# Performance work log

Hardware: AMD Instinct MI355X
Metric: run time of the kernel (lower is better)

Reference implementation:

```python
import jax, jax.numpy as jnp
import numpy as np

WS = 8
NH = 6

def _ln(x, g, b, eps=1e-5):
    m = x.mean(-1, keepdims=True)
    v = jnp.var(x, axis=-1, keepdims=True)
    return (x - m) / jnp.sqrt(v + eps) * g + b

def _dwconv(x_nchw, k):
    # depthwise 3x3, stride 1, padding 1 (SAME); k: (C,1,3,3)
    return jax.lax.conv_general_dilated(
        x_nchw, k, (1, 1), 'SAME',
        dimension_numbers=('NCHW', 'OIHW', 'NCHW'),
        feature_group_count=x_nchw.shape[1])

def setup_inputs() -> dict:
    key = jax.random.key(0)
    ks = jax.random.split(key, 12)
    B, H, W, C = 2, 256, 256, 180
    hd_ffn = 360
    s = 0.02
    return {
        'x': jax.random.normal(ks[0], (B, H * W, C), jnp.float32),
        'w_qkv': jax.random.normal(ks[1], (3 * C, C), jnp.float32) * s,
        'b_rel': jax.random.normal(ks[2], (NH, WS * WS, WS * WS), jnp.float32) * s,
        'w_proj': jax.random.normal(ks[3], (C, C), jnp.float32) * s,
        'b_proj': jnp.zeros((C,), jnp.float32),
        'conv_dw': jax.random.normal(ks[4], (C, 1, 3, 3), jnp.float32) * 0.1,
        'cg_w1': jax.random.normal(ks[5], (C // 8, C), jnp.float32) * s,
        'cg_w2': jax.random.normal(ks[6], (C, C // 8), jnp.float32) * s,
        'ffn_w1': jax.random.normal(ks[7], (hd_ffn, C), jnp.float32) * s,
        'ffn_dw': jax.random.normal(ks[8], (hd_ffn, 1, 3, 3), jnp.float32) * 0.1,
        'ffn_w2': jax.random.normal(ks[9], (C, hd_ffn), jnp.float32) * s,
        'n1_g': jnp.ones((C,), jnp.float32),
        'n1_b': jnp.zeros((C,), jnp.float32),
        'n2_g': jnp.ones((C,), jnp.float32),
        'n2_b': jnp.zeros((C,), jnp.float32),
        'H': H,
        'W': W,
    }

def reference(x, w_qkv, b_rel, w_proj, b_proj, conv_dw, cg_w1, cg_w2,
              ffn_w1, ffn_dw, ffn_w2, n1_g, n1_b, n2_g, n2_b, H, W):
    B, L, C = x.shape
    hd = C // NH
    scale = hd ** -0.5
    n1 = _ln(x, n1_g, n1_b)
    # --- spatial window attention branch ---
    xw = n1.reshape(B, H // WS, WS, W // WS, WS, C)
    xw = xw.transpose(0, 1, 3, 2, 4, 5).reshape(-1, WS * WS, C)  # (nw, 64, C)
    qkv = (xw @ w_qkv.T).reshape(-1, WS * WS, 3, NH, hd).transpose(2, 0, 3, 1, 4)
    q, k, v = qkv[0], qkv[1], qkv[2]  # (nw, nh, 64, hd)
    attn = jax.nn.softmax((q * scale) @ jnp.swapaxes(k, -2, -1) + b_rel, axis=-1)
    out = (attn @ v).transpose(0, 2, 1, 3).reshape(-1, WS * WS, C)
    out = out @ w_proj.T + b_proj
    attn_feat = out.reshape(B, H // WS, W // WS, WS, WS, C)
    attn_feat = attn_feat.transpose(0, 1, 3, 2, 4, 5).reshape(B, L, C)
    # --- conv branch: depthwise 3x3 + GELU ---
    nchw = n1.transpose(0, 2, 1).reshape(B, C, H, W)
    conv_feat = jax.nn.gelu(_dwconv(nchw, conv_dw), approximate=False)
    conv_feat = conv_feat.reshape(B, C, L).transpose(0, 2, 1)
    # --- AIM: channel gate on conv_feat modulates attn_feat ---
    pooled = conv_feat.mean(axis=1)  # (B, C) == AdaptiveAvgPool2d(1)
    cm = jax.nn.sigmoid(jax.nn.gelu(pooled @ cg_w1.T, approximate=False) @ cg_w2.T)
    x = x + (attn_feat * cm[:, None, :] + conv_feat)
    # --- FFN with depthwise spatial mixing ---
    n2 = _ln(x, n2_g, n2_b)
    h = jax.nn.gelu(n2 @ ffn_w1.T, approximate=False)  # (B, L, hd_ffn)
    hdim = h.shape[-1]
    h_s = _dwconv(h.transpose(0, 2, 1).reshape(B, hdim, H, W), ffn_dw)
    h_s = h_s.reshape(B, hdim, L).transpose(0, 2, 1)
    return x + h_s @ ffn_w2.T
```

## Files before the change

### kernel.cpp

```cpp
#include <hip/hip_runtime.h>
#include <hip/hip_bf16.h>
#include <math.h>

#define BATCH 2
#define IMG 256
#define LTOK 65536
#define CH 180
#define BL (BATCH * LTOK)
#define HDF 360

using frag_ab = __attribute__((ext_vector_type(8))) short;
using frag_cd = __attribute__((ext_vector_type(4))) float;

__device__ __forceinline__ float b2f(unsigned short u) {
    union { unsigned int i; float f; } v; v.i = ((unsigned int)u) << 16; return v.f;
}
__device__ __forceinline__ float blo(unsigned int u) {
    union { unsigned int i; float f; } v; v.i = u << 16; return v.f;
}
__device__ __forceinline__ float bhi(unsigned int u) {
    union { unsigned int i; float f; } v; v.i = u & 0xffff0000u; return v.f;
}
__device__ __forceinline__ unsigned short f2b(float f) {
    union { float f; unsigned int i; } v; v.f = f;
    unsigned int x = v.i;
    unsigned int r = (x + 0x7fffu + ((x >> 16) & 1u)) >> 16;
    return (unsigned short)r;
}
__device__ __forceinline__ float gelu_f(float x) {
    return 0.5f * x * (1.0f + erff(x * 0.70710678118654752f));
}

__global__ __launch_bounds__(256) void convw_kernel(
    const float* __restrict__ a, const float* __restrict__ b,
    const float* __restrict__ c, const float* __restrict__ d,
    const float* __restrict__ cdw, const float* __restrict__ fdw,
    unsigned short* __restrict__ wbf, float* __restrict__ wT1, float* __restrict__ wT2)
{
    int g = blockIdx.x * 256 + threadIdx.x;
    if (g < 259200) {
        float v;
        if      (g < 97200)  v = a[g];
        else if (g < 129600) v = b[g - 97200];
        else if (g < 194400) v = c[g - 129600];
        else                 v = d[g - 194400];
        wbf[g] = f2b(v);
    } else if (g < 265680) {
        int i = g - 259200;
        int tap = i / 180, ch = i % 180;
        wT1[i] = cdw[ch * 9 + tap];
    } else if (g < 278640) {
        int i = g - 265680;
        int tap = i / 360, ch = i % 360;
        wT2[i] = fdw[ch * 9 + tap];
    }
}

__device__ __forceinline__ void ld4(const float* p, float v[4]) {
    float4 t = *(const float4*)p; v[0]=t.x; v[1]=t.y; v[2]=t.z; v[3]=t.w;
}
__device__ __forceinline__ void ld4(const unsigned short* p, float v[4]) {
    ushort4 t = *(const ushort4*)p; v[0]=b2f(t.x); v[1]=b2f(t.y); v[2]=b2f(t.z); v[3]=b2f(t.w);
}

template <typename TIN>
__global__ __launch_bounds__(256) void ln_kernel(
    const TIN* __restrict__ x, const float* __restrict__ g,
    const float* __restrict__ bta, unsigned short* __restrict__ out)
{
    int wave = threadIdx.x >> 6, lane = threadIdx.x & 63;
    int tok = blockIdx.x * 4 + wave;
    const bool act = lane < 45;
    float v[4] = {0.f, 0.f, 0.f, 0.f};
    const TIN* row = x + (size_t)tok * CH;
    if (act) ld4(row + lane * 4, v);
    float s  = v[0] + v[1] + v[2] + v[3];
    float sq = v[0]*v[0] + v[1]*v[1] + v[2]*v[2] + v[3]*v[3];
    #pragma unroll
    for (int off = 32; off > 0; off >>= 1) {
        s  += __shfl_xor(s, off);
        sq += __shfl_xor(sq, off);
    }
    float mean = s * (1.f / CH);
    float var  = sq * (1.f / CH) - mean * mean;
    float rstd = rsqrtf(var + 1e-5f);
    if (act) {
        float4 gg = *(const float4*)&g[lane * 4];
        float4 bb = *(const float4*)&bta[lane * 4];
        unsigned int o0 = (unsigned int)f2b((v[0]-mean)*rstd*gg.x + bb.x)
                        | ((unsigned int)f2b((v[1]-mean)*rstd*gg.y + bb.y) << 16);
        unsigned int o1 = (unsigned int)f2b((v[2]-mean)*rstd*gg.z + bb.z)
                        | ((unsigned int)f2b((v[3]-mean)*rstd*gg.w + bb.w) << 16);
        *(uint2*)(out + (size_t)tok * CH + lane * 4) = make_uint2(o0, o1);
    }
}

__device__ __forceinline__ void stv(float* p, float v) { *p = v; }
__device__ __forceinline__ void stv(unsigned short* p, float v) { *p = f2b(v); }

template <int ACT, bool HAS_BIAS, bool HAS_RES, typename TOUT>
__global__ __launch_bounds__(256) void gemm_kernel(
    const unsigned short* __restrict__ X, int ldx,
    const unsigned short* __restrict__ Wt,
    const float* __restrict__ bias,
    const unsigned short* __restrict__ res, int ldr,
    TOUT* __restrict__ Y, int ldy,
    int N, int K)
{
    __shared__ unsigned short Xs[64][40];
    __shared__ unsigned short Ws[64][40];
    const int tid = threadIdx.x;
    const int wave = tid >> 6;
    const int lane = tid & 63;
    const int l16 = lane & 15;
    const int q = lane >> 4;
    const int m0 = blockIdx.x * 64;
    const int n0 = blockIdx.y * 64;
    const int lr = tid >> 2;
    const int lk = (tid & 3) << 3;

    frag_cd acc[4];
    #pragma unroll
    for (int i = 0; i < 4; ++i) acc[i] = (frag_cd){0.f, 0.f, 0.f, 0.f};

    for (int k0 = 0; k0 < K; k0 += 32) {
        const bool kfull = (k0 + 32 <= K);
        {
            const unsigned short* p = X + (size_t)(m0 + lr) * ldx + (k0 + lk);
            if (kfull) {
                *(uint2*)&Xs[lr][lk]     = *(const uint2*)p;
                *(uint2*)&Xs[lr][lk + 4] = *(const uint2*)(p + 4);
            } else {
                #pragma unroll
                for (int j = 0; j < 8; ++j)
                    Xs[lr][lk + j] = (k0 + lk + j < K) ? p[j] : (unsigned short)0;
            }
        }
        {
            const int n = n0 + lr;
            const unsigned short* p = Wt + (size_t)n * K + (k0 + lk);
            if (n < N && kfull) {
                *(uint2*)&Ws[lr][lk]     = *(const uint2*)p;
                *(uint2*)&Ws[lr][lk + 4] = *(const uint2*)(p + 4);
            } else {
                #pragma unroll
                for (int j = 0; j < 8; ++j)
                    Ws[lr][lk + j] = (n < N && (k0 + lk + j) < K) ? p[j] : (unsigned short)0;
            }
        }
        __syncthreads();
        frag_ab bfr = *(const frag_ab*)&Ws[wave * 16 + l16][q * 8];
        #pragma unroll
        for (int mb = 0; mb < 4; ++mb) {
            frag_ab afr = *(const frag_ab*)&Xs[mb * 16 + l16][q * 8];
            acc[mb] = __builtin_amdgcn_mfma_f32_16x16x32_bf16(afr, bfr, acc[mb], 0, 0, 0);
        }
        __syncthreads();
    }
    const int col = n0 + wave * 16 + l16;
    if (col < N) {
        float bv = 0.f;
        if (HAS_BIAS) bv = bias[col];
        #pragma unroll
        for (int mb = 0; mb < 4; ++mb) {
            #pragma unroll
            for (int r = 0; r < 4; ++r) {
                int row = m0 + mb * 16 + q * 4 + r;
                float v = acc[mb][r] + bv;
                if (ACT == 1) v = gelu_f(v);
                if (HAS_RES) v += b2f(res[(size_t)row * ldr + col]);
                stv(&Y[(size_t)row * ldy + col], v);
            }
        }
    }
}

__global__ __launch_bounds__(256) void attn_kernel(
    const unsigned short* __restrict__ qkv,
    const float* __restrict__ b_rel,
    unsigned short* __restrict__ attn_out)
{
    __shared__ float qs[64][33], ks[64][33], vs[64][33];
    __shared__ float S[64][65];
    const int tid = threadIdx.x;
    const int wid = blockIdx.x;
    const int b = wid >> 10;
    const int wy = (wid & 1023) >> 5;
    const int wx = wid & 31;
    const float scale = 0.18257418583505536f;
    const int ty = tid >> 4, tx = tid & 15;

    for (int h = 0; h < 6; ++h) {
        for (int idx = tid; idx < 64 * 32; idx += 256) {
            int r = idx >> 5, d = idx & 31;
            float qv = 0.f, kv = 0.f, vv = 0.f;
            if (d < 30) {
                int l = ((wy << 3) + (r >> 3)) * IMG + (wx << 3) + (r & 7);
                const unsigned short* rowp = qkv + (size_t)(b * LTOK + l) * 540 + h * 30 + d;
                qv = b2f(rowp[0]); kv = b2f(rowp[180]); vv = b2f(rowp[360]);
            }
            qs[r][d] = qv; ks[r][d] = kv; vs[r][d] = vv;
        }
        __syncthreads();
        {
            float a4[4][4] = {{0.f}};
            for (int d = 0; d < 30; ++d) {
                float qv[4], kv[4];
                #pragma unroll
                for (int i = 0; i < 4; ++i) qv[i] = qs[ty * 4 + i][d];
                #pragma unroll
                for (int j = 0; j < 4; ++j) kv[j] = ks[tx * 4 + j][d];
                #pragma unroll
                for (int i = 0; i < 4; ++i)
                    #pragma unroll
                    for (int j = 0; j < 4; ++j) a4[i][j] += qv[i] * kv[j];
            }
            #pragma unroll
            for (int i = 0; i < 4; ++i)
                #pragma unroll
                for (int j = 0; j < 4; ++j) {
                    int ii = ty * 4 + i, jj = tx * 4 + j;
                    S[ii][jj] = a4[i][j] * scale + b_rel[h * 4096 + ii * 64 + jj];
                }
        }
        __syncthreads();
        if (tid < 64) {
            float mx = -1e30f;
            for (int j = 0; j < 64; ++j) mx = fmaxf(mx, S[tid][j]);
            float sum = 0.f;
            for (int j = 0; j < 64; ++j) { float e = __expf(S[tid][j] - mx); S[tid][j] = e; sum += e; }
            float inv = 1.f / sum;
            for (int j = 0; j < 64; ++j) S[tid][j] *= inv;
        }
        __syncthreads();
        {
            const int i0 = ty * 4, d0 = tx * 2;
            float o[4][2] = {{0.f}};
            for (int j = 0; j < 64; ++j) {
                float v0 = vs[j][d0], v1 = vs[j][d0 + 1];
                #pragma unroll
                for (int i = 0; i < 4; ++i) {
                    float p = S[i0 + i][j];
                    o[i][0] += p * v0;
                    o[i][1] += p * v1;
                }
            }
            if (d0 < 30) {
                #pragma unroll
                for (int i = 0; i < 4; ++i) {
                    int r = i0 + i;
                    int l = ((wy << 3) + (r >> 3)) * IMG + (wx << 3) + (r & 7);
                    unsigned short* op = attn_out + (size_t)(b * LTOK + l) * CH + h * 30 + d0;
                    op[0] = f2b(o[i][0]);
                    op[1] = f2b(o[i][1]);
                }
            }
        }
        __syncthreads();
    }
}

template <int C, bool DO_GELU>
__global__ __launch_bounds__(256) void dwconv_kernel(
    const unsigned short* __restrict__ in, const float* __restrict__ wT,
    unsigned short* __restrict__ out)
{
    constexpr int NG = (C + 7) / 8;
    constexpr int TY = 8;
    int gid = blockIdx.x * 256 + threadIdx.x;
    int cg = gid % NG;
    int t  = gid / NG;
    int x  = t % IMG;
    int t2 = t / IMG;
    int yb = t2 & 31;
    int bi = t2 >> 5;
    if (bi >= BATCH) return;
    const int c0 = cg * 8;
    const int y0 = yb * TY;

    float w9[9][8];
    #pragma unroll
    for (int tp = 0; tp < 9; ++tp) {
        float4 wa = *(const float4*)&wT[tp * C + c0];
        float4 wb = *(const float4*)&wT[tp * C + c0 + 4];
        w9[tp][0]=wa.x; w9[tp][1]=wa.y; w9[tp][2]=wa.z; w9[tp][3]=wa.w;
        w9[tp][4]=wb.x; w9[tp][5]=wb.y; w9[tp][6]=wb.z; w9[tp][7]=wb.w;
    }

    unsigned int rr[3][3][4];

    auto load_row = [&](int y, unsigned int dst[3][4]) {
        if ((unsigned)y >= (unsigned)IMG) {
            #pragma unroll
            for (int cc = 0; cc < 3; ++cc)
                #pragma unroll
                for (int k = 0; k < 4; ++k) dst[cc][k] = 0u;
            return;
        }
        size_t base = ((size_t)((bi << 16) + (y << 8) + x)) * C + c0;
        #pragma unroll
        for (int cc = 0; cc < 3; ++cc) {
            int xx = x + cc - 1;
            if ((unsigned)xx >= (unsigned)IMG) {
                dst[cc][0] = dst[cc][1] = dst[cc][2] = dst[cc][3] = 0u;
                continue;
            }
            const unsigned short* p = in + base + (ptrdiff_t)(cc - 1) * C;
            uint2 u0 = *(const uint2*)p;
            uint2 u1 = *(const uint2*)(p + 4);
            dst[cc][0] = u0.x; dst[cc][1] = u0.y; dst[cc][2] = u1.x; dst[cc][3] = u1.y;
        }
    };

    load_row(y0 - 1, rr[0]);
    load_row(y0,     rr[1]);

    #pragma unroll
    for (int dy = 0; dy < TY; ++dy) {
        load_row(y0 + dy + 1, rr[(dy + 2) % 3]);
        float acc[8];
        #pragma unroll
        for (int j = 0; j < 8; ++j) acc[j] = 0.f;
        #pragma unroll
        for (int ky = 0; ky < 3; ++ky) {
            unsigned int (*row)[4] = rr[(dy + ky) % 3];
            #pragma unroll
            for (int kx = 0; kx < 3; ++kx) {
                const float* wp = w9[ky * 3 + kx];
                const unsigned int* u = row[kx];
                acc[0] += blo(u[0]) * wp[0];
                acc[1] += bhi(u[0]) * wp[1];
                acc[2] += blo(u[1]) * wp[2];
                acc[3] += bhi(u[1]) * wp[3];
                acc[4] += blo(u[2]) * wp[4];
                acc[5] += bhi(u[2]) * wp[5];
                acc[6] += blo(u[3]) * wp[6];
                acc[7] += bhi(u[3]) * wp[7];
            }
        }
        if (DO_GELU) {
            #pragma unroll
            for (int j = 0; j < 8; ++j) acc[j] = gelu_f(acc[j]);
        }
        size_t ob = ((size_t)((bi << 16) + ((y0 + dy) << 8) + x)) * C + c0;
        unsigned int o0 = (unsigned int)f2b(acc[0]) | ((unsigned int)f2b(acc[1]) << 16);
        unsigned int o1 = (unsigned int)f2b(acc[2]) | ((unsigned int)f2b(acc[3]) << 16);
        *(uint2*)(out + ob) = make_uint2(o0, o1);
        if (c0 + 8 <= C) {
            unsigned int o2 = (unsigned int)f2b(acc[4]) | ((unsigned int)f2b(acc[5]) << 16);
            unsigned int o3 = (unsigned int)f2b(acc[6]) | ((unsigned int)f2b(acc[7]) << 16);
            *(uint2*)(out + ob + 4) = make_uint2(o2, o3);
        }
    }
}

__global__ __launch_bounds__(64) void pool_kernel(
    const unsigned short* __restrict__ cf, float* __restrict__ pooled)
{
    int t = threadIdx.x;
    if (t >= 45) return;
    int b = blockIdx.x >> 7;
    int chunk = blockIdx.x & 127;
    const unsigned short* base = cf + (size_t)(b * LTOK + chunk * 512) * CH + t * 4;
    float s0 = 0.f, s1 = 0.f, s2 = 0.f, s3 = 0.f;
    for (int i = 0; i < 512; ++i) {
        ushort4 v = *(const ushort4*)(base + (size_t)i * CH);
        s0 += b2f(v.x); s1 += b2f(v.y); s2 += b2f(v.z); s3 += b2f(v.w);
    }
    atomicAdd(&pooled[b * CH + t * 4 + 0], s0);
    atomicAdd(&pooled[b * CH + t * 4 + 1], s1);
    atomicAdd(&pooled[b * CH + t * 4 + 2], s2);
    atomicAdd(&pooled[b * CH + t * 4 + 3], s3);
}

__global__ __launch_bounds__(256) void cm_kernel(
    const float* __restrict__ pooled, const float* __restrict__ w1,
    const float* __restrict__ w2, float* __restrict__ cm)
{
    __shared__ float p[BATCH][CH];
    __shared__ float g1[BATCH][22];
    int t = threadIdx.x;
    for (int idx = t; idx < BATCH * CH; idx += 256)
        p[idx / CH][idx % CH] = pooled[idx] * (1.f / (float)LTOK);
    __syncthreads();
    if (t < BATCH * 22) {
        int b = t / 22, u = t % 22;
        float s = 0.f;
        for (int c = 0; c < CH; ++c) s += p[b][c] * w1[u * CH + c];
        g1[b][u] = gelu_f(s);
    }
    __syncthreads();
    for (int idx = t; idx < BATCH * CH; idx += 256) {
        int b = idx / CH, c = idx % CH;
        float s = 0.f;
        for (int u = 0; u < 22; ++u) s += g1[b][u] * w2[c * 22 + u];
        cm[idx] = 1.f / (1.f + __expf(-s));
    }
}

__global__ __launch_bounds__(256) void resid_kernel(
    const float* __restrict__ x, const unsigned short* __restrict__ attn_feat,
    const unsigned short* __restrict__ conv_feat, const float* __restrict__ cm,
    unsigned short* __restrict__ x_mid)
{
    int gid = blockIdx.x * 256 + threadIdx.x;
    int c4 = gid % 45;
    int b = gid / (LTOK * 45);
    float4 xv = ((const float4*)x)[gid];
    ushort4 a = ((const ushort4*)attn_feat)[gid];
    ushort4 c = ((const ushort4*)conv_feat)[gid];
    float4 m = *(const float4*)&cm[b * CH + c4 * 4];
    unsigned int o0 = (unsigned int)f2b(xv.x + b2f(a.x) * m.x + b2f(c.x))
                    | ((unsigned int)f2b(xv.y + b2f(a.y) * m.y + b2f(c.y)) << 16);
    unsigned int o1 = (unsigned int)f2b(xv.z + b2f(a.z) * m.z + b2f(c.z))
                    | ((unsigned int)f2b(xv.w + b2f(a.w) * m.w + b2f(c.w)) << 16);
    ((uint2*)x_mid)[gid] = make_uint2(o0, o1);
}

extern "C" void kernel_launch(void* const* d_in, const int* in_sizes, int n_in,
                              void* d_out, int out_size, void* d_ws, size_t ws_size,
                              hipStream_t stream)
{
    const float* x       = (const float*)d_in[0];
    const float* w_qkv   = (const float*)d_in[1];
    const float* b_rel   = (const float*)d_in[2];
    const float* w_proj  = (const float*)d_in[3];
    const float* b_proj  = (const float*)d_in[4];
    const float* conv_dw = (const float*)d_in[5];
    const float* cg_w1   = (const float*)d_in[6];
    const float* cg_w2   = (const float*)d_in[7];
    const float* ffn_w1  = (const float*)d_in[8];
    const float* ffn_dw  = (const float*)d_in[9];
    const float* ffn_w2  = (const float*)d_in[10];
    const float* n1_g    = (const float*)d_in[11];
    const float* n1_b    = (const float*)d_in[12];
    const float* n2_g    = (const float*)d_in[13];
    const float* n2_b    = (const float*)d_in[14];

    char* ws = (char*)d_ws;
    unsigned short* n1        = (unsigned short*)(ws);
    unsigned short* qkv       = (unsigned short*)(ws + 47185920);
    unsigned short* conv_feat = (unsigned short*)(ws + 188743680);
    unsigned short* attn_out  = (unsigned short*)(ws);
    unsigned short* attn_feat = (unsigned short*)(ws + 47185920);
    unsigned short* x_mid     = (unsigned short*)(ws + 94371840);
    unsigned short* n2        = (unsigned short*)(ws + 141557760);
    unsigned short* h         = (unsigned short*)(ws);
    unsigned short* h_s       = (unsigned short*)(ws + 141557760);
    float*          pooled    = (float*)(ws + 235929600);
    float*          cmv       = (float*)(ws + 235931040);
    unsigned short* wbf       = (unsigned short*)(ws + 235932480);
    float*          wT1       = (float*)(ws + 236450880);
    float*          wT2       = (float*)(ws + 236476800);
    unsigned short* wqkv_b  = wbf;
    unsigned short* wproj_b = wbf + 97200;
    unsigned short* wffn1_b = wbf + 129600;
    unsigned short* wffn2_b = wbf + 194400;
    float* out = (float*)d_out;

    hipMemsetAsync(pooled, 0, 2880, stream);

    convw_kernel<<<1089, 256, 0, stream>>>(w_qkv, w_proj, ffn_w1, ffn_w2,
                                           conv_dw, ffn_dw, wbf, wT1, wT2);
    ln_kernel<float><<<BL / 4, 256, 0, stream>>>(x, n1_g, n1_b, n1);
    gemm_kernel<0, false, false, unsigned short><<<dim3(BL / 64, 9), 256, 0, stream>>>(
        n1, CH, wqkv_b, nullptr, nullptr, 0, qkv, 540, 540, CH);
    dwconv_kernel<CH, true><<<1472, 256, 0, stream>>>(n1, wT1, conv_feat);
    pool_kernel<<<BATCH * 128, 64, 0, stream>>>(conv_feat, pooled);
    cm_kernel<<<1, 256, 0, stream>>>(pooled, cg_w1, cg_w2, cmv);
    attn_kernel<<<2048, 256, 0, stream>>>(qkv, b_rel, attn_out);
    gemm_kernel<0, true, false, unsigned short><<<dim3(BL / 64, 3), 256, 0, stream>>>(
        attn_out, CH, wproj_b, b_proj, nullptr, 0, attn_feat, CH, CH, CH);
    resid_kernel<<<(BL * CH / 4) / 256, 256, 0, stream>>>(x, attn_feat, conv_feat, cmv, x_mid);
    ln_kernel<unsigned short><<<BL / 4, 256, 0, stream>>>(x_mid, n2_g, n2_b, n2);
    gemm_kernel<1, false, false, unsigned short><<<dim3(BL / 64, 6), 256, 0, stream>>>(
        n2, CH, wffn1_b, nullptr, nullptr, 0, h, HDF, HDF, CH);
    dwconv_kernel<HDF, false><<<2880, 256, 0, stream>>>(h, wT2, h_s);
    gemm_kernel<0, false, true, float><<<dim3(BL / 64, 3), 256, 0, stream>>>(
        h_s, HDF, wffn2_b, nullptr, x_mid, CH, out, CH, CH, HDF);
}
```

Baseline: 1.111 ms.

## Store QKV in window-major layout and rewrite attention as one-thread-per-query

The QKV GEMM epilogue now scatters rows into a window-major order, so each window's 64 tokens are contiguous. The projection GEMM un-permutes the rows back to image order on store. The attention kernel becomes one 64-thread block per (window, head), with each thread holding its query row, score row and output in registers and K/V staged in LDS. This targets the strided gathers, multiple block-wide barriers and shared-memory S traffic of the old kernel, at the cost of heavy register use (scores plus q and o arrays) and scattered GEMM stores.

New measurement: 1.064 ms. -4.3%, faster.

```diff
diff --git a/kernel.cpp b/kernel.cpp
--- a/kernel.cpp
+++ b/kernel.cpp
@@ -29,6 +29,21 @@
 }
 __device__ __forceinline__ float gelu_f(float x) {
     return 0.5f * x * (1.0f + erff(x * 0.70710678118654752f));
+}
+
+template <int PERM>
+__device__ __forceinline__ int perm_row(int row) {
+    if (PERM == 1) {
+        int b = row >> 16, l = row & 65535;
+        int y = l >> 8, x = l & 255;
+        return (b << 16) + ((((y >> 3) << 5) + (x >> 3)) << 6) + ((y & 7) << 3) + (x & 7);
+    } else if (PERM == 2) {
+        int b = row >> 16, wv = row & 65535;
+        int wid = wv >> 6, t = wv & 63;
+        int wy = wid >> 5, wx = wid & 31;
+        return (b << 16) + ((((wy << 3) + (t >> 3))) << 8) + (wx << 3) + (t & 7);
+    }
+    return row;
 }
 
 __global__ __launch_bounds__(256) void convw_kernel(
@@ -98,7 +113,7 @@
 __device__ __forceinline__ void stv(float* p, float v) { *p = v; }
 __device__ __forceinline__ void stv(unsigned short* p, float v) { *p = f2b(v); }
 
-template <int ACT, bool HAS_BIAS, bool HAS_RES, typename TOUT>
+template <int ACT, bool HAS_BIAS, bool HAS_RES, int PERM, typename TOUT>
 __global__ __launch_bounds__(256) void gemm_kernel(
     const unsigned short* __restrict__ X, int ldx,
     const unsigned short* __restrict__ Wt,
@@ -166,97 +181,86 @@
             #pragma unroll
             for (int r = 0; r < 4; ++r) {
                 int row = m0 + mb * 16 + q * 4 + r;
+                int orow = perm_row<PERM>(row);
                 float v = acc[mb][r] + bv;
                 if (ACT == 1) v = gelu_f(v);
-                if (HAS_RES) v += b2f(res[(size_t)row * ldr + col]);
-                stv(&Y[(size_t)row * ldy + col], v);
+                if (HAS_RES) v += b2f(res[(size_t)orow * ldr + col]);
+                stv(&Y[(size_t)orow * ldy + col], v);
             }
         }
     }
 }
 
-__global__ __launch_bounds__(256) void attn_kernel(
-    const unsigned short* __restrict__ qkv,
+__global__ __launch_bounds__(64) void attn_kernel(
+    const unsigned short* __restrict__ qkvw,
     const float* __restrict__ b_rel,
     unsigned short* __restrict__ attn_out)
 {
-    __shared__ float qs[64][33], ks[64][33], vs[64][33];
-    __shared__ float S[64][65];
-    const int tid = threadIdx.x;
-    const int wid = blockIdx.x;
-    const int b = wid >> 10;
-    const int wy = (wid & 1023) >> 5;
-    const int wx = wid & 31;
+    __shared__ float kv[64][36];
+    const int blk = blockIdx.x;
+    const int h = blk % 6;
+    const int w = blk / 6;
+    const int lane = threadIdx.x;
     const float scale = 0.18257418583505536f;
-    const int ty = tid >> 4, tx = tid & 15;
-
-    for (int h = 0; h < 6; ++h) {
-        for (int idx = tid; idx < 64 * 32; idx += 256) {
-            int r = idx >> 5, d = idx & 31;
-            float qv = 0.f, kv = 0.f, vv = 0.f;
-            if (d < 30) {
-                int l = ((wy << 3) + (r >> 3)) * IMG + (wx << 3) + (r & 7);
-                const unsigned short* rowp = qkv + (size_t)(b * LTOK + l) * 540 + h * 30 + d;
-                qv = b2f(rowp[0]); kv = b2f(rowp[180]); vv = b2f(rowp[360]);
-            }
-            qs[r][d] = qv; ks[r][d] = kv; vs[r][d] = vv;
-        }
-        __syncthreads();
-        {
-            float a4[4][4] = {{0.f}};
-            for (int d = 0; d < 30; ++d) {
-                float qv[4], kv[4];
-                #pragma unroll
-                for (int i = 0; i < 4; ++i) qv[i] = qs[ty * 4 + i][d];
-                #pragma unroll
-                for (int j = 0; j < 4; ++j) kv[j] = ks[tx * 4 + j][d];
-                #pragma unroll
-                for (int i = 0; i < 4; ++i)
-                    #pragma unroll
-                    for (int j = 0; j < 4; ++j) a4[i][j] += qv[i] * kv[j];
-            }
-            #pragma unroll
-            for (int i = 0; i < 4; ++i)
-                #pragma unroll
-                for (int j = 0; j < 4; ++j) {
-                    int ii = ty * 4 + i, jj = tx * 4 + j;
-                    S[ii][jj] = a4[i][j] * scale + b_rel[h * 4096 + ii * 64 + jj];
-                }
-        }
-        __syncthreads();
-        if (tid < 64) {
-            float mx = -1e30f;
-            for (int j = 0; j < 64; ++j) mx = fmaxf(mx, S[tid][j]);
-            float sum = 0.f;
-            for (int j = 0; j < 64; ++j) { float e = __expf(S[tid][j] - mx); S[tid][j] = e; sum += e; }
-            float inv = 1.f / sum;
-            for (int j = 0; j < 64; ++j) S[tid][j] *= inv;
-        }
-        __syncthreads();
-        {
-            const int i0 = ty * 4, d0 = tx * 2;
-            float o[4][2] = {{0.f}};
-            for (int j = 0; j < 64; ++j) {
-                float v0 = vs[j][d0], v1 = vs[j][d0 + 1];
-                #pragma unroll
-                for (int i = 0; i < 4; ++i) {
-                    float p = S[i0 + i][j];
-                    o[i][0] += p * v0;
-                    o[i][1] += p * v1;
-                }
-            }
-            if (d0 < 30) {
-                #pragma unroll
-                for (int i = 0; i < 4; ++i) {
-                    int r = i0 + i;
-                    int l = ((wy << 3) + (r >> 3)) * IMG + (wx << 3) + (r & 7);
-                    unsigned short* op = attn_out + (size_t)(b * LTOK + l) * CH + h * 30 + d0;
-                    op[0] = f2b(o[i][0]);
-                    op[1] = f2b(o[i][1]);
-                }
-            }
-        }
-        __syncthreads();
+
+    const unsigned short* qrow = qkvw + (size_t)(w * 64 + lane) * 540 + h * 30;
+
+    float q[30];
+    #pragma unroll
+    for (int d = 0; d < 15; ++d) {
+        unsigned int u = *(const unsigned int*)(qrow + 2 * d);
+        q[2 * d] = blo(u); q[2 * d + 1] = bhi(u);
+    }
+    #pragma unroll
+    for (int d = 0; d < 15; ++d) {
+        unsigned int u = *(const unsigned int*)(qrow + 180 + 2 * d);
+        kv[lane][2 * d] = blo(u); kv[lane][2 * d + 1] = bhi(u);
+    }
+    __syncthreads();
+
+    float s[64];
+    const float* br = b_rel + h * 4096 + lane * 64;
+    #pragma unroll
+    for (int j = 0; j < 64; ++j) {
+        const float* kj = &kv[j][0];
+        float acc = 0.f;
+        #pragma unroll
+        for (int d = 0; d < 30; ++d) acc += q[d] * kj[d];
+        s[j] = acc * scale + br[j];
+    }
+
+    float mx = -1e30f;
+    #pragma unroll
+    for (int j = 0; j < 64; ++j) mx = fmaxf(mx, s[j]);
+    float sum = 0.f;
+    #pragma unroll
+    for (int j = 0; j < 64; ++j) { s[j] = __expf(s[j] - mx); sum += s[j]; }
+    float inv = 1.f / sum;
+
+    __syncthreads();
+    #pragma unroll
+    for (int d = 0; d < 15; ++d) {
+        unsigned int u = *(const unsigned int*)(qrow + 360 + 2 * d);
+        kv[lane][2 * d] = blo(u); kv[lane][2 * d + 1] = bhi(u);
+    }
+    __syncthreads();
+
+    float o[30];
+    #pragma unroll
+    for (int d = 0; d < 30; ++d) o[d] = 0.f;
+    #pragma unroll
+    for (int j = 0; j < 64; ++j) {
+        const float* vj = &kv[j][0];
+        float p = s[j];
+        #pragma unroll
+        for (int d = 0; d < 30; ++d) o[d] += p * vj[d];
+    }
+    unsigned short* orow = attn_out + (size_t)(w * 64 + lane) * CH + h * 30;
+    #pragma unroll
+    for (int d = 0; d < 15; ++d) {
+        unsigned int u = (unsigned int)f2b(o[2 * d] * inv)
+                       | ((unsigned int)f2b(o[2 * d + 1] * inv) << 16);
+        *(unsigned int*)(orow + 2 * d) = u;
     }
 }
 
@@ -439,7 +443,7 @@
 
     char* ws = (char*)d_ws;
     unsigned short* n1        = (unsigned short*)(ws);
-    unsigned short* qkv       = (unsigned short*)(ws + 47185920);
+    unsigned short* qkvw      = (unsigned short*)(ws + 47185920);
     unsigned short* conv_feat = (unsigned short*)(ws + 188743680);
     unsigned short* attn_out  = (unsigned short*)(ws);
     unsigned short* attn_feat = (unsigned short*)(ws + 47185920);
@@ -463,19 +467,19 @@
     convw_kernel<<<1089, 256, 0, stream>>>(w_qkv, w_proj, ffn_w1, ffn_w2,
                                            conv_dw, ffn_dw, wbf, wT1, wT2);
     ln_kernel<float><<<BL / 4, 256, 0, stream>>>(x, n1_g, n1_b, n1);
-    gemm_kernel<0, false, false, unsigned short><<<dim3(BL / 64, 9), 256, 0, stream>>>(
-        n1, CH, wqkv_b, nullptr, nullptr, 0, qkv, 540, 540, CH);
+    gemm_kernel<0, false, false, 1, unsigned short><<<dim3(BL / 64, 9), 256, 0, stream>>>(
+        n1, CH, wqkv_b, nullptr, nullptr, 0, qkvw, 540, 540, CH);
     dwconv_kernel<CH, true><<<1472, 256, 0, stream>>>(n1, wT1, conv_feat);
     pool_kernel<<<BATCH * 128, 64, 0, stream>>>(conv_feat, pooled);
     cm_kernel<<<1, 256, 0, stream>>>(pooled, cg_w1, cg_w2, cmv);
-    attn_kernel<<<2048, 256, 0, stream>>>(qkv, b_rel, attn_out);
-    gemm_kernel<0, true, false, unsigned short><<<dim3(BL / 64, 3), 256, 0, stream>>>(
+    attn_kernel<<<2048 * 6, 64, 0, stream>>>(qkvw, b_rel, attn_out);
+    gemm_kernel<0, true, false, 2, unsigned short><<<dim3(BL / 64, 3), 256, 0, stream>>>(
         attn_out, CH, wproj_b, b_proj, nullptr, 0, attn_feat, CH, CH, CH);
     resid_kernel<<<(BL * CH / 4) / 256, 256, 0, stream>>>(x, attn_feat, conv_feat, cmv, x_mid);
     ln_kernel<unsigned short><<<BL / 4, 256, 0, stream>>>(x_mid, n2_g, n2_b, n2);
-    gemm_kernel<1, false, false, unsigned short><<<dim3(BL / 64, 6), 256, 0, stream>>>(
+    gemm_kernel<1, false, false, 0, unsigned short><<<dim3(BL / 64, 6), 256, 0, stream>>>(
         n2, CH, wffn1_b, nullptr, nullptr, 0, h, HDF, HDF, CH);
     dwconv_kernel<HDF, false><<<2880, 256, 0, stream>>>(h, wT2, h_s);
-    gemm_kernel<0, false, true, float><<<dim3(BL / 64, 3), 256, 0, stream>>>(
+    gemm_kernel<0, false, true, 0, float><<<dim3(BL / 64, 3), 256, 0, stream>>>(
         h_s, HDF, wffn2_b, nullptr, x_mid, CH, out, CH, CH, HDF);
 }
```
